# Kernel optimization log

Measured on AMD Instinct MI355X. Metric: run time of the kernel, lower is better.

## Reference

```python
import jax, jax.numpy as jnp
import numpy as np

N = 20000      # nodes
E = 320000     # edges (before self loops)
IN = 128       # in_channels
H = 8          # heads
C = 33         # hidden per head
D = H * C      # 264, concat width
OUT = D // 2   # 132, readout width
NEG_SLOPE = 0.2


def setup_inputs() -> dict:
    key = jax.random.key(0)
    ks = jax.random.split(key, 24)
    inp = {}
    inp["x"] = jax.random.normal(ks[0], (N, IN), jnp.float32)
    inp["edge_index"] = jax.random.randint(ks[1], (2, E), 0, N, dtype=jnp.int32)
    in_dims = [IN, D, D, D]
    k = 2
    for i, din in enumerate(in_dims):
        s = 1.0 / np.sqrt(din)
        inp[f"W{i}"] = jax.random.normal(ks[k], (din, D), jnp.float32) * s; k += 1
        inp[f"a_src{i}"] = jax.random.normal(ks[k], (H, C), jnp.float32) * 0.1; k += 1
        inp[f"a_dst{i}"] = jax.random.normal(ks[k], (H, C), jnp.float32) * 0.1; k += 1
        inp[f"b{i}"] = jnp.zeros((D,), jnp.float32)
    inp["W_head"] = jax.random.normal(ks[k], (D, OUT), jnp.float32) * (1.0 / np.sqrt(D)); k += 1
    inp["b_head"] = jnp.zeros((OUT,), jnp.float32)
    return inp


def _gat_layer(h, src, dst, W, a_s, a_d, b):
    # h: [N, din] -> out: [N, H*C]
    xh = (h @ W).reshape(-1, H, C)                  # [N, H, C]
    alpha_s = jnp.sum(xh * a_s, axis=-1)            # [N, H]
    alpha_d = jnp.sum(xh * a_d, axis=-1)            # [N, H]
    e = jax.nn.leaky_relu(alpha_s[src] + alpha_d[dst], NEG_SLOPE)  # [E', H]
    # segment softmax over incoming edges per destination node
    m = jax.ops.segment_max(e, dst, num_segments=N)                # [N, H]
    ex = jnp.exp(e - m[dst])
    denom = jax.ops.segment_sum(ex, dst, num_segments=N)           # [N, H]
    alpha = ex / (denom[dst] + 1e-16)                              # [E', H]
    msg = xh[src] * alpha[..., None]                               # [E', H, C]
    out = jax.ops.segment_sum(msg, dst, num_segments=N)            # [N, H, C]
    return out.reshape(-1, D) + b


def reference(x, edge_index, W0, a_src0, a_dst0, b0, W1, a_src1, a_dst1, b1,
              W2, a_src2, a_dst2, b2, W3, a_src3, a_dst3, b3, W_head, b_head):
    # PyG GATConv default add_self_loops=True
    loops = jnp.arange(N, dtype=edge_index.dtype)
    src = jnp.concatenate([edge_index[0], loops])
    dst = jnp.concatenate([edge_index[1], loops])
    params = [(W0, a_src0, a_dst0, b0), (W1, a_src1, a_dst1, b1),
              (W2, a_src2, a_dst2, b2), (W3, a_src3, a_dst3, b3)]
    h = x
    for (W, a_s, a_d, b) in params:
        h = _gat_layer(h, src, dst, W, a_s, a_d, b)
        h = jax.nn.elu(h)
    z = h @ W_head + b_head  # readout (dropout off at inference)
    return z
```

## Files before the change

### kernel.cpp

```cpp
#include <hip/hip_runtime.h>
#include <hip/hip_bf16.h>

#define N_NODES 20000
#define N_EDGES 320000
#define TOT_E   (N_EDGES + N_NODES)
#define IN_CH   128
#define HEADS   8
#define CH      33
#define DD      264
#define OUTW    132
#define NEG     0.2f

#define LDB     272
#define LDA     320
#define NT_HID  18
#define NT_HEAD 12
#define PK0     4
#define PKH     10
#define PKO     10

typedef unsigned short ushort;
typedef unsigned int uint32;
typedef short bf16x8 __attribute__((ext_vector_type(8)));
typedef float f32x4  __attribute__((ext_vector_type(4)));

__device__ inline void split2(float v, ushort& hi, ushort& lo) {
    __hip_bfloat16 h = __float2bfloat16(v);
    float r = v - __bfloat162float(h);
    __hip_bfloat16 l = __float2bfloat16(r);
    hi = *(ushort*)&h;
    lo = *(ushort*)&l;
}

__device__ inline float bf2f(ushort u) {
    union { unsigned int i; float f; } c;
    c.i = ((unsigned int)u) << 16;
    return c.f;
}

__device__ inline float bflo(uint32 d) {
    union { unsigned int i; float f; } c;
    c.i = d << 16;
    return c.f;
}
__device__ inline float bfhi(uint32 d) {
    union { unsigned int i; float f; } c;
    c.i = d & 0xffff0000u;
    return c.f;
}


__global__ void deg_k(const int* __restrict__ ei, int* __restrict__ deg) {
    int e = blockIdx.x * 256 + threadIdx.x;
    if (e >= TOT_E) return;
    int dst = (e < N_EDGES) ? ei[N_EDGES + e] : (e - N_EDGES);
    atomicAdd(&deg[dst], 1);
}

__global__ __launch_bounds__(1024) void scan_k(const int* __restrict__ deg,
                                               int* __restrict__ rowp) {
    __shared__ int part[1024];
    const int PER = 20;
    int t = threadIdx.x;
    int base = t * PER;
    int s = 0;
    for (int i = 0; i < PER; ++i) {
        int idx = base + i;
        if (idx < N_NODES) s += deg[idx];
    }
    part[t] = s;
    __syncthreads();
    for (int off = 1; off < 1024; off <<= 1) {
        int v = 0;
        if (t >= off) v = part[t - off];
        __syncthreads();
        part[t] += v;
        __syncthreads();
    }
    int run = part[t] - s;
    for (int i = 0; i < PER; ++i) {
        int idx = base + i;
        if (idx < N_NODES) { rowp[idx] = run; run += deg[idx]; }
    }
    if (t == 1023) rowp[N_NODES] = part[1023];
}

__global__ void fill_k(const int* __restrict__ ei, const int* __restrict__ rowp,
                       int* __restrict__ cur, int* __restrict__ csr) {
    int e = blockIdx.x * 256 + threadIdx.x;
    if (e >= TOT_E) return;
    int src, dst;
    if (e < N_EDGES) { src = ei[e]; dst = ei[N_EDGES + e]; }
    else             { src = dst = e - N_EDGES; }
    int p = atomicAdd(&cur[dst], 1);
    csr[rowp[dst] + p] = src;
}


__global__ void splitx_k(const float* __restrict__ x, ushort* __restrict__ ahi) {
    int idx = blockIdx.x * 256 + threadIdx.x;
    if (idx >= N_NODES * IN_CH) return;
    int n = idx >> 7, k = idx & 127;
    __hip_bfloat16 h = __float2bfloat16(x[idx]);
    ahi[(size_t)n * LDA + k] = *(ushort*)&h;
}


__device__ void convw_one(const float* W, const float* a_s, const float* a_d,
                          int K, int NC, int NT, ushort* fhi, ushort* flo, int gid) {
    int p = gid / (NT * 64);
    int rem = gid % (NT * 64);
    int t = rem >> 6, c = rem & 63;
    int kq = c >> 4, m = c & 15;
    int n = t * 16 + m;
    bool stats = (a_s != nullptr) && (t == NT - 1);
    ushort hi8[8], lo8[8];
#pragma unroll
    for (int j = 0; j < 8; ++j) {
        int k = p * 32 + kq * 8 + j;
        float v = 0.f;
        if (k < K) {
            if (stats) {
                const float* av = (m < 8) ? a_s : a_d;
                int h = (m < 8) ? m : m - 8;
                const float* wr = W + (size_t)k * NC + h * CH;
                float s = 0.f;
                for (int cc = 0; cc < CH; ++cc) s += wr[cc] * av[h * CH + cc];
                v = s;
            } else if (n < NC) {
                v = W[(size_t)k * NC + n];
            }
        }
        split2(v, hi8[j], lo8[j]);
    }
    size_t o = ((size_t)gid) * 8;
#pragma unroll
    for (int j = 0; j < 8; ++j) { fhi[o + j] = hi8[j]; flo[o + j] = lo8[j]; }
}

#define SEG0 (PK0 * NT_HID * 64)
#define SEGH (PKH * NT_HID * 64)
#define SEGO (PKO * NT_HEAD * 64)

__global__ void convall_k(
    const float* W0, const float* W1, const float* W2, const float* W3, const float* Wh,
    const float* as0, const float* as1, const float* as2, const float* as3,
    const float* ad0, const float* ad1, const float* ad2, const float* ad3,
    ushort* f0h, ushort* f0l, ushort* f1h, ushort* f1l, ushort* f2h, ushort* f2l,
    ushort* f3h, ushort* f3l, ushort* fhh, ushort* fhl) {
    int gid = blockIdx.x * 256 + threadIdx.x;
    if (gid < SEG0) { convw_one(W0, as0, ad0, IN_CH, DD, NT_HID, f0h, f0l, gid); return; }
    gid -= SEG0;
    if (gid < SEGH) { convw_one(W1, as1, ad1, DD, DD, NT_HID, f1h, f1l, gid); return; }
    gid -= SEGH;
    if (gid < SEGH) { convw_one(W2, as2, ad2, DD, DD, NT_HID, f2h, f2l, gid); return; }
    gid -= SEGH;
    if (gid < SEGH) { convw_one(W3, as3, ad3, DD, DD, NT_HID, f3h, f3l, gid); return; }
    gid -= SEGH;
    if (gid < SEGO) { convw_one(Wh, nullptr, nullptr, DD, OUTW, NT_HEAD, fhh, fhl, gid); }
}


template<bool USE3, int TG>
__global__ __launch_bounds__(256) void gemm4_k(
    const ushort* __restrict__ Ahi, const ushort* __restrict__ Alo, int kpairs,
    const ushort* __restrict__ Bhi, const ushort* __restrict__ Blo, int NTtot, int statsY,
    ushort* __restrict__ Cb16, float* __restrict__ as_, float* __restrict__ ad_,
    float* __restrict__ C, int ldc, int ncguard, const float* __restrict__ bias) {
    extern __shared__ ushort smem[];
    ushort* AlH = smem;
    ushort* BlH = smem + 8192;
    ushort* EXT = smem + 8192 + 2 * TG * 512;
    ushort* AlL = EXT;
    ushort* BlL = EXT + 8192;
    ushort* BstL = EXT;

    int tid = threadIdx.x;
    int m0 = blockIdx.x * 128;
    int t0 = blockIdx.y * TG;
    bool sg = ((int)blockIdx.y == statsY);

    f32x4 acc[2][TG];
#pragma unroll
    for (int mt = 0; mt < 2; ++mt)
#pragma unroll
        for (int t = 0; t < TG; ++t) acc[mt][t] = (f32x4){0.f, 0.f, 0.f, 0.f};

    int w = tid >> 6, lane = tid & 63;
    int csA = (lane ^ ((lane >> 4) << 1)) * 8;

    for (int pp = 0; pp < kpairs; ++pp) {
        int nA = USE3 ? 2048 : 1024;
        for (int id = tid; id < nA; id += 256) {
            int hl = id >> 10;
            int cid = id & 1023;
            int mrow = cid >> 3, kq8 = cid & 7;
            int panel = kq8 >> 2, kq = kq8 & 3;
            int gm = m0 + mrow;
            uint4 v = {0, 0, 0, 0};
            if (gm < N_NODES) {
                const ushort* src = (hl ? Alo : Ahi) + (size_t)gm * LDA + pp * 64 + kq8 * 8;
                v = *(const uint4*)src;
            }
            int c = kq * 16 + (mrow & 15);
            int cs = c ^ ((c >> 4) << 1);
            ushort* dst = (hl ? AlL : AlH) + panel * 4096 + (mrow >> 4) * 512 + cs * 8;
            *(uint4*)dst = v;
        }
        for (int id = tid; id < 2 * TG * 64; id += 256) {
            int c = id & 63;
            int r = id >> 6;
            int t = r % TG;
            int panel = r / TG;
            const ushort* src = Bhi + ((size_t)((pp * 2 + panel) * NTtot + t0 + t) * 64 + c) * 8;
            *(uint4*)&BlH[(panel * TG + t) * 512 + c * 8] = *(const uint4*)src;
        }
        if (USE3) {
            for (int id = tid; id < 2 * TG * 64; id += 256) {
                int c = id & 63;
                int r = id >> 6;
                int t = r % TG;
                int panel = r / TG;
                const ushort* src = Blo + ((size_t)((pp * 2 + panel) * NTtot + t0 + t) * 64 + c) * 8;
                *(uint4*)&BlL[(panel * TG + t) * 512 + c * 8] = *(const uint4*)src;
            }
        } else if (sg) {
            for (int id = tid; id < 2 * 64; id += 256) {
                int c = id & 63;
                int panel = id >> 6;
                const ushort* src = Blo + ((size_t)((pp * 2 + panel) * NTtot + t0 + TG - 1) * 64 + c) * 8;
                *(uint4*)&BstL[panel * 512 + c * 8] = *(const uint4*)src;
            }
        }
        __syncthreads();

#pragma unroll
        for (int panel = 0; panel < 2; ++panel) {
            bf16x8 a0 = *(const bf16x8*)&AlH[panel * 4096 + (2 * w) * 512 + csA];
            bf16x8 a1 = *(const bf16x8*)&AlH[panel * 4096 + (2 * w + 1) * 512 + csA];
            bf16x8 l0, l1;
            if (USE3) {
                l0 = *(const bf16x8*)&AlL[panel * 4096 + (2 * w) * 512 + csA];
                l1 = *(const bf16x8*)&AlL[panel * 4096 + (2 * w + 1) * 512 + csA];
            }
#pragma unroll
            for (int t = 0; t < TG; ++t) {
                bf16x8 bh = *(const bf16x8*)&BlH[(panel * TG + t) * 512 + lane * 8];
                acc[0][t] = __builtin_amdgcn_mfma_f32_16x16x32_bf16(a0, bh, acc[0][t], 0, 0, 0);
                acc[1][t] = __builtin_amdgcn_mfma_f32_16x16x32_bf16(a1, bh, acc[1][t], 0, 0, 0);
                if (USE3) {
                    bf16x8 bl = *(const bf16x8*)&BlL[(panel * TG + t) * 512 + lane * 8];
                    acc[0][t] = __builtin_amdgcn_mfma_f32_16x16x32_bf16(a0, bl, acc[0][t], 0, 0, 0);
                    acc[1][t] = __builtin_amdgcn_mfma_f32_16x16x32_bf16(a1, bl, acc[1][t], 0, 0, 0);
                    acc[0][t] = __builtin_amdgcn_mfma_f32_16x16x32_bf16(l0, bh, acc[0][t], 0, 0, 0);
                    acc[1][t] = __builtin_amdgcn_mfma_f32_16x16x32_bf16(l1, bh, acc[1][t], 0, 0, 0);
                } else if (t == TG - 1 && sg) {
                    bf16x8 bst = *(const bf16x8*)&BstL[panel * 512 + lane * 8];
                    acc[0][t] = __builtin_amdgcn_mfma_f32_16x16x32_bf16(a0, bst, acc[0][t], 0, 0, 0);
                    acc[1][t] = __builtin_amdgcn_mfma_f32_16x16x32_bf16(a1, bst, acc[1][t], 0, 0, 0);
                }
            }
        }
        __syncthreads();
    }

    int col = lane & 15;
#pragma unroll
    for (int mt = 0; mt < 2; ++mt) {
        int rbase = m0 + (2 * w + mt) * 16 + ((lane >> 4) << 2);
#pragma unroll
        for (int t = 0; t < TG; ++t) {
            int tg = t0 + t;
#pragma unroll
            for (int r = 0; r < 4; ++r) {
                int gm = rbase + r;
                if (gm >= N_NODES) continue;
                float v = acc[mt][t][r];
                if (C) {
                    int gn = tg * 16 + col;
                    if (gn < ncguard) C[(size_t)gm * ldc + gn] = v + bias[gn];
                } else if (tg < 17) {
                    __hip_bfloat16 bv = __float2bfloat16(v);
                    Cb16[(size_t)gm * LDB + tg * 16 + col] = *(ushort*)&bv;
                } else {
                    if (col < 8) as_[(size_t)gm * 8 + col] = v;
                    else         ad_[(size_t)gm * 8 + col - 8] = v;
                }
            }
        }
    }
}


__global__ __launch_bounds__(64) void gat_k(
    const ushort* __restrict__ xb, const float* __restrict__ as_,
    const float* __restrict__ ad_, const int* __restrict__ rowp,
    const int* __restrict__ csr, const float* __restrict__ bias,
    ushort* __restrict__ outhi, ushort* __restrict__ outlo) {
    int lane = threadIdx.x;
    int half = lane >> 5, l32 = lane & 31;
    int node = blockIdx.x * 2 + half;
    int r0 = rowp[node], dg = rowp[node + 1] - r0;

    __shared__ float lex[2][32][9];
    __shared__ int   lsrc[2][32];

    float ad[8];
#pragma unroll
    for (int h = 0; h < 8; ++h) ad[h] = ad_[node * 8 + h];

    int cb = l32 * 8;
    int ha = cb / 33;
    int hb = (cb + 7) / 33;
    bool mm[8];
#pragma unroll
    for (int j = 0; j < 8; ++j) mm[j] = ((cb + j) / 33) != ha;

    float a0[8];
#pragma unroll
    for (int j = 0; j < 8; ++j) a0[j] = 0.f;
    float a1[4] = {0.f, 0.f, 0.f, 0.f};
    float sm[8] = {0.f, 0.f, 0.f, 0.f, 0.f, 0.f, 0.f, 0.f};

    int mych = (dg + 31) >> 5;
    int och = __shfl_xor(mych, 32, 64);
    int maxch = mych > och ? mych : och;

    for (int c = 0; c < maxch; ++c) {
        int base = c << 5, j = base + l32;
        int s = node;
        float p8[8];
#pragma unroll
        for (int h = 0; h < 8; ++h) p8[h] = 0.f;
        if (j < dg) {
            s = csr[r0 + j];
            const float* ap = as_ + (size_t)s * 8;
#pragma unroll
            for (int h = 0; h < 8; ++h) {
                float e = ap[h] + ad[h];
                e = e > 0.f ? e : NEG * e;
                float p = __expf(e);
                p8[h] = p;
                sm[h] += p;
            }
        }
        lsrc[half][l32] = s * LDB;
#pragma unroll
        for (int h = 0; h < 8; ++h) lex[half][l32][h] = p8[h];
        __builtin_amdgcn_wave_barrier();

        int rem = dg - base;
        int cnt = rem < 0 ? 0 : (rem > 32 ? 32 : rem);
        int cnt4 = (cnt + 3) & ~3;
        for (int jj = 0; jj < cnt4; jj += 4) {
            int o0 = lsrc[half][jj + 0], o1 = lsrc[half][jj + 1];
            int o2 = lsrc[half][jj + 2], o3 = lsrc[half][jj + 3];
            const uint4* p0 = (const uint4*)(xb + (size_t)(unsigned)o0);
            const uint4* p1 = (const uint4*)(xb + (size_t)(unsigned)o1);
            const uint4* p2 = (const uint4*)(xb + (size_t)(unsigned)o2);
            const uint4* p3 = (const uint4*)(xb + (size_t)(unsigned)o3);
            uint4 v0 = p0[l32], v1 = p1[l32], v2 = p2[l32], v3 = p3[l32];
            const uint2* q0 = (const uint2*)p0;
            const uint2* q1 = (const uint2*)p1;
            const uint2* q2 = (const uint2*)p2;
            const uint2* q3 = (const uint2*)p3;
            uint2 t0 = q0[64 + (l32 & 1)], t1 = q1[64 + (l32 & 1)];
            uint2 t2 = q2[64 + (l32 & 1)], t3 = q3[64 + (l32 & 1)];
#pragma unroll
            for (int e = 0; e < 4; ++e) {
                const float* xr = lex[half][jj + e];
                float xa = xr[ha], xbv = xr[hb], x7 = xr[7];
                uint4 v = (e == 0) ? v0 : (e == 1) ? v1 : (e == 2) ? v2 : v3;
                uint2 t = (e == 0) ? t0 : (e == 1) ? t1 : (e == 2) ? t2 : t3;
                a0[0] += (mm[0] ? xbv : xa) * bflo(v.x);
                a0[1] += (mm[1] ? xbv : xa) * bfhi(v.x);
                a0[2] += (mm[2] ? xbv : xa) * bflo(v.y);
                a0[3] += (mm[3] ? xbv : xa) * bfhi(v.y);
                a0[4] += (mm[4] ? xbv : xa) * bflo(v.z);
                a0[5] += (mm[5] ? xbv : xa) * bfhi(v.z);
                a0[6] += (mm[6] ? xbv : xa) * bflo(v.w);
                a0[7] += (mm[7] ? xbv : xa) * bfhi(v.w);
                a1[0] += x7 * bflo(t.x);
                a1[1] += x7 * bfhi(t.x);
                a1[2] += x7 * bflo(t.y);
                a1[3] += x7 * bfhi(t.y);
            }
        }
        __builtin_amdgcn_wave_barrier();
    }

    float iv[8];
#pragma unroll
    for (int h = 0; h < 8; ++h) {
        float s = sm[h];
        for (int off = 16; off; off >>= 1) s += __shfl_xor(s, off, 64);
        iv[h] = 1.0f / (s + 1e-16f);
    }

    {
        float iva = iv[ha], ivb = iv[hb];
        ushort hi8[8], lo8[8];
        float4 b0 = *(const float4*)(bias + cb);
        float4 b1 = *(const float4*)(bias + cb + 4);
        float bv4[8] = {b0.x, b0.y, b0.z, b0.w, b1.x, b1.y, b1.z, b1.w};
#pragma unroll
        for (int j = 0; j < 8; ++j) {
            float v = a0[j] * (mm[j] ? ivb : iva) + bv4[j];
            v = v > 0.f ? v : (__expf(v) - 1.f);
            split2(v, hi8[j], lo8[j]);
        }
        size_t o = (size_t)node * LDA + cb;
        *(ushort4*)(outhi + o) = *(ushort4*)&hi8[0];
        *(ushort4*)(outhi + o + 4) = *(ushort4*)&hi8[4];
        if (outlo) {
            *(ushort4*)(outlo + o) = *(ushort4*)&lo8[0];
            *(ushort4*)(outlo + o + 4) = *(ushort4*)&lo8[4];
        }
    }
    if (l32 < 2) {
        ushort hi4[4], lo4[4];
        float4 bt = *(const float4*)(bias + 256 + l32 * 4);
        float bv4[4] = {bt.x, bt.y, bt.z, bt.w};
#pragma unroll
        for (int j = 0; j < 4; ++j) {
            float v = a1[j] * iv[7] + bv4[j];
            v = v > 0.f ? v : (__expf(v) - 1.f);
            split2(v, hi4[j], lo4[j]);
        }
        size_t o = (size_t)node * LDA + 256 + l32 * 4;
        *(ushort4*)(outhi + o) = *(ushort4*)hi4;
        if (outlo) *(ushort4*)(outlo + o) = *(ushort4*)lo4;
    } else if (l32 < 9) {
        ushort4 z = {0, 0, 0, 0};
        size_t o = (size_t)node * LDA + 264 + (l32 - 2) * 8;
        *(ushort4*)(outhi + o) = z;
        *(ushort4*)(outhi + o + 4) = z;
        if (outlo) {
            *(ushort4*)(outlo + o) = z;
            *(ushort4*)(outlo + o + 4) = z;
        }
    }
}


extern "C" void kernel_launch(void* const* d_in, const int* in_sizes, int n_in,
                              void* d_out, int out_size, void* d_ws, size_t ws_size,
                              hipStream_t stream) {
    const float* x  = (const float*)d_in[0];
    const int*   ei = (const int*)d_in[1];
    const float* W[4]  = {(const float*)d_in[2],  (const float*)d_in[6],
                          (const float*)d_in[10], (const float*)d_in[14]};
    const float* As[4] = {(const float*)d_in[3],  (const float*)d_in[7],
                          (const float*)d_in[11], (const float*)d_in[15]};
    const float* Ad[4] = {(const float*)d_in[4],  (const float*)d_in[8],
                          (const float*)d_in[12], (const float*)d_in[16]};
    const float* Bb[4] = {(const float*)d_in[5],  (const float*)d_in[9],
                          (const float*)d_in[13], (const float*)d_in[17]};
    const float* Wh = (const float*)d_in[18];
    const float* bh = (const float*)d_in[19];

    char* p = (char*)d_ws;
    ushort* hBb  = (ushort*)p;          p += (size_t)N_NODES * LDB * 2;
    ushort* hAhi = (ushort*)p;          p += (size_t)N_NODES * LDA * 2;
    ushort* hAlo = (ushort*)p;          p += (size_t)N_NODES * LDA * 2;
    float* as_  = (float*)p;            p += (size_t)N_NODES * HEADS * 4;
    float* ad_  = (float*)p;            p += (size_t)N_NODES * HEADS * 4;
    const int wsz0 = PK0 * NT_HID * 512;
    const int wszH = PKH * NT_HID * 512;
    const int wszO = PKO * NT_HEAD * 512;
    ushort* wfhi[4]; ushort* wflo[4];
    for (int l = 0; l < 4; ++l) {
        int sz = (l == 0) ? wsz0 : wszH;
        wfhi[l] = (ushort*)p; p += (size_t)sz * 2;
        wflo[l] = (ushort*)p; p += (size_t)sz * 2;
    }
    ushort* whhi = (ushort*)p; p += (size_t)wszO * 2;
    ushort* whlo = (ushort*)p; p += (size_t)wszO * 2;
    int* deg  = (int*)p;  p += N_NODES * 4;
    int* cur  = (int*)p;  p += N_NODES * 4;
    int* rowp = (int*)p;  p += (N_NODES + 1) * 4;
    int* csr  = (int*)p;  p += (size_t)TOT_E * 4;

    hipMemsetAsync(deg, 0, sizeof(int) * 2 * N_NODES, stream);
    int egrid = (TOT_E + 255) / 256;
    deg_k<<<egrid, 256, 0, stream>>>(ei, deg);
    scan_k<<<1, 1024, 0, stream>>>(deg, rowp);
    fill_k<<<egrid, 256, 0, stream>>>(ei, rowp, cur, csr);

    splitx_k<<<(N_NODES * IN_CH + 255) / 256, 256, 0, stream>>>(x, hAhi);
    {
        int tot = SEG0 + 3 * SEGH + SEGO;
        convall_k<<<(tot + 255) / 256, 256, 0, stream>>>(
            W[0], W[1], W[2], W[3], Wh,
            As[0], As[1], As[2], As[3],
            Ad[0], Ad[1], Ad[2], Ad[3],
            wfhi[0], wflo[0], wfhi[1], wflo[1], wfhi[2], wflo[2],
            wfhi[3], wflo[3], whhi, whlo);
    }

    dim3 gG((N_NODES + 127) / 128, NT_HID / 6);
    dim3 gO((N_NODES + 127) / 128, NT_HEAD / 6);
    size_t smHid = (size_t)(8192 + 2 * 6 * 512 + 2 * 512) * 2;
    size_t smHead = (size_t)(8192 + 2 * 6 * 512 + 8192 + 2 * 6 * 512) * 2;

    for (int l = 0; l < 4; ++l) {
        int kpairs = (l == 0) ? PK0 / 2 : PKH / 2;
        gemm4_k<false, 6><<<gG, 256, smHid, stream>>>(hAhi, nullptr, kpairs,
                                                      wfhi[l], wflo[l], NT_HID, 2,
                                                      hBb, as_, ad_, nullptr, 0, 0, nullptr);
        gat_k<<<N_NODES / 2, 64, 0, stream>>>(hBb, as_, ad_, rowp, csr, Bb[l],
                                              hAhi, (l == 3) ? hAlo : nullptr);
    }

    gemm4_k<true, 6><<<gO, 256, smHead, stream>>>(hAhi, hAlo, PKO / 2,
                                                  whhi, whlo, NT_HEAD, -1,
                                                  nullptr, nullptr, nullptr,
                                                  (float*)d_out, OUTW, OUTW, bh);
}
```

Before: 417.1 us.

## Load GEMM tiles directly into LDS and linearize grid for tile locality

Replaces the register-staged global-to-LDS copies of the A and B tiles in the GEMM kernel with global_load_lds direct transfers, 16 bytes per lane, with each wave filling one 512-element LDS chunk. Out-of-range A rows are clamped to the last node instead of being zero-filled. The 2D grid is flattened into 1D so that consecutive blocks share the same row tile across column groups, which should improve L2 reuse of A. This removes the VGPR round-trip and the per-element address math on loads. In exchange it relies on the swizzled layout matching the lane order of the direct-to-LDS writes, and the clamped rows only produce garbage in rows that should be discarded.

New measurement: 385.9 us. 1.08x faster.

```diff
diff --git a/kernel.cpp b/kernel.cpp
--- a/kernel.cpp
+++ b/kernel.cpp
@@ -47,6 +47,12 @@
     union { unsigned int i; float f; } c;
     c.i = d & 0xffff0000u;
     return c.f;
+}
+
+__device__ __forceinline__ void ld_lds16(const ushort* g, ushort* l) {
+    __builtin_amdgcn_global_load_lds(
+        (const __attribute__((address_space(1))) void*)g,
+        (__attribute__((address_space(3))) void*)l, 16, 0, 0);
 }
 
 
@@ -176,9 +182,11 @@
     ushort* BstL = EXT;
 
     int tid = threadIdx.x;
-    int m0 = blockIdx.x * 128;
-    int t0 = blockIdx.y * TG;
-    bool sg = ((int)blockIdx.y == statsY);
+    int ngy = NTtot / TG;
+    int m0 = (blockIdx.x / ngy) * 128;
+    int by = blockIdx.x % ngy;
+    int t0 = by * TG;
+    bool sg = (by == statsY);
 
     f32x4 acc[2][TG];
 #pragma unroll
@@ -189,48 +197,31 @@
     int w = tid >> 6, lane = tid & 63;
     int csA = (lane ^ ((lane >> 4) << 1)) * 8;
 
+    int kqA = lane >> 4;
+    int m15 = (lane ^ (kqA << 1)) & 15;
+
     for (int pp = 0; pp < kpairs; ++pp) {
-        int nA = USE3 ? 2048 : 1024;
-        for (int id = tid; id < nA; id += 256) {
-            int hl = id >> 10;
-            int cid = id & 1023;
-            int mrow = cid >> 3, kq8 = cid & 7;
-            int panel = kq8 >> 2, kq = kq8 & 3;
-            int gm = m0 + mrow;
-            uint4 v = {0, 0, 0, 0};
-            if (gm < N_NODES) {
-                const ushort* src = (hl ? Alo : Ahi) + (size_t)gm * LDA + pp * 64 + kq8 * 8;
-                v = *(const uint4*)src;
-            }
-            int c = kq * 16 + (mrow & 15);
-            int cs = c ^ ((c >> 4) << 1);
-            ushort* dst = (hl ? AlL : AlH) + panel * 4096 + (mrow >> 4) * 512 + cs * 8;
-            *(uint4*)dst = v;
-        }
-        for (int id = tid; id < 2 * TG * 64; id += 256) {
-            int c = id & 63;
-            int r = id >> 6;
-            int t = r % TG;
-            int panel = r / TG;
-            const ushort* src = Bhi + ((size_t)((pp * 2 + panel) * NTtot + t0 + t) * 64 + c) * 8;
-            *(uint4*)&BlH[(panel * TG + t) * 512 + c * 8] = *(const uint4*)src;
-        }
-        if (USE3) {
-            for (int id = tid; id < 2 * TG * 64; id += 256) {
-                int c = id & 63;
-                int r = id >> 6;
-                int t = r % TG;
-                int panel = r / TG;
-                const ushort* src = Blo + ((size_t)((pp * 2 + panel) * NTtot + t0 + t) * 64 + c) * 8;
-                *(uint4*)&BlL[(panel * TG + t) * 512 + c * 8] = *(const uint4*)src;
-            }
-        } else if (sg) {
-            for (int id = tid; id < 2 * 64; id += 256) {
-                int c = id & 63;
-                int panel = id >> 6;
-                const ushort* src = Blo + ((size_t)((pp * 2 + panel) * NTtot + t0 + TG - 1) * 64 + c) * 8;
-                *(uint4*)&BstL[panel * 512 + c * 8] = *(const uint4*)src;
-            }
+        int nArows = USE3 ? 32 : 16;
+        for (int r = w; r < nArows; r += 4) {
+            int hl = r >> 4;
+            int panel = (r >> 3) & 1;
+            int mrow16 = r & 7;
+            int gm = m0 + mrow16 * 16 + m15;
+            if (gm > N_NODES - 1) gm = N_NODES - 1;
+            const ushort* g = (hl ? Alo : Ahi) + (size_t)gm * LDA + pp * 64 + panel * 32 + kqA * 8;
+            ushort* l = (hl ? AlL : AlH) + (panel * 8 + mrow16) * 512;
+            ld_lds16(g, l);
+        }
+        for (int r = w; r < 2 * TG; r += 4) {
+            int panel = r / TG, t = r % TG;
+            size_t row = (size_t)((pp * 2 + panel) * NTtot + t0 + t) * 512;
+            ld_lds16(Bhi + row + lane * 8, &BlH[r * 512]);
+            if (USE3) ld_lds16(Blo + row + lane * 8, &BlL[r * 512]);
+        }
+        if (!USE3 && sg && w < 2) {
+            int panel = w;
+            size_t row = (size_t)((pp * 2 + panel) * NTtot + t0 + TG - 1) * 512;
+            ld_lds16(Blo + row + lane * 8, &BstL[panel * 512]);
         }
         __syncthreads();
 
@@ -498,8 +489,9 @@
             wfhi[3], wflo[3], whhi, whlo);
     }
 
-    dim3 gG((N_NODES + 127) / 128, NT_HID / 6);
-    dim3 gO((N_NODES + 127) / 128, NT_HEAD / 6);
+    int nmb = (N_NODES + 127) / 128;
+    int gG = nmb * (NT_HID / 6);
+    int gO = nmb * (NT_HEAD / 6);
     size_t smHid = (size_t)(8192 + 2 * 6 * 512 + 2 * 512) * 2;
     size_t smHead = (size_t)(8192 + 2 * 6 * 512 + 8192 + 2 * 6 * 512) * 2;
 
```
